# Kernel optimization log

Hardware: AMD Instinct MI355X
Metric: run time of the kernel (lower is better)

Reference implementation:

```python
import jax, jax.numpy as jnp
import numpy as np

STATE_DIM = 64
HIDDEN_DIM = 256
BATCH = 4096
DT = 0.01


def setup_inputs() -> dict:
    key = jax.random.key(0)
    ks = jax.random.split(key, 7)
    s = 1.0 / np.sqrt(STATE_DIM)
    h = 1.0 / np.sqrt(HIDDEN_DIM)
    return {
        "x0": jax.random.normal(ks[0], (BATCH, STATE_DIM), dtype=jnp.float32),
        "W1": jax.random.uniform(ks[1], (STATE_DIM, HIDDEN_DIM), jnp.float32, -s, s),
        "b1": jax.random.uniform(ks[2], (HIDDEN_DIM,), jnp.float32, -s, s),
        "W2": jax.random.uniform(ks[3], (HIDDEN_DIM, HIDDEN_DIM), jnp.float32, -h, h),
        "b2": jax.random.uniform(ks[4], (HIDDEN_DIM,), jnp.float32, -h, h),
        "W3": jax.random.uniform(ks[5], (HIDDEN_DIM, STATE_DIM), jnp.float32, -h, h),
        "b3": jax.random.uniform(ks[6], (STATE_DIM,), jnp.float32, -h, h),
        "dt_scale": jnp.ones((1,), dtype=jnp.float32) * 0.01,
        "steps": 200,
    }


def reference(x0, W1, b1, W2, b2, W3, b3, dt_scale, steps):
    def func(x):
        h1 = jnp.tanh(x @ W1 + b1)
        h2 = jnp.tanh(h1 @ W2 + b2)
        return h2 @ W3 + b3

    def step(x, _):
        x_next = x + func(x) * dt_scale * DT  # Euler update
        return x_next, x_next

    _, traj = jax.lax.scan(step, x0, None, length=steps)
    # traj: [steps, batch, state_dim] -> [batch, steps+1, state_dim]
    return jnp.concatenate([x0[:, None, :], jnp.swapaxes(traj, 0, 1)], axis=1)
```

## Files before the change

kernel.cpp:

```cpp
#include <hip/hip_runtime.h>


#define STATE_DIM 64
#define HIDDEN    256
#define BATCH     4096
#define TILE_M    16
#define NBLK      (BATCH / TILE_M)
#define XPITCH    72
#define HPITCH    264

typedef short v8s __attribute__((ext_vector_type(8)));
typedef float v4f __attribute__((ext_vector_type(4)));

__device__ __forceinline__ unsigned short f2bf(float f) {
    unsigned u = __float_as_uint(f);
    u += 0x7fffu + ((u >> 16) & 1u);
    return (unsigned short)(u >> 16);
}

__device__ __forceinline__ float fast_tanh(float x) {
    float e = __builtin_amdgcn_exp2f(x * 2.8853900817779268f);
    return 1.0f - 2.0f * __builtin_amdgcn_rcpf(e + 1.0f);
}

__global__ void prep_weights(const float* __restrict__ W1,
                             const float* __restrict__ W2,
                             const float* __restrict__ W3,
                             short* __restrict__ W1t,
                             short* __restrict__ W2t,
                             short* __restrict__ W3t) {
    int u = blockIdx.x * 256 + threadIdx.x;
    if (u < 65536) {
        int n = u >> 8, k = u & 255;
        W2t[u] = (short)f2bf(W2[k * 256 + n]);
    }
    int v = u - 65536;
    if (v >= 0 && v < 16384) {
        int n = v >> 6, k = v & 63;
        W1t[v] = (short)f2bf(W1[k * 256 + n]);
    }
    int t = u - (65536 + 16384);
    if (t >= 0 && t < 16384) {
        int n = t >> 8, k = t & 255;
        W3t[t] = (short)f2bf(W3[k * 64 + n]);
    }
}

__global__ __launch_bounds__(512, 2)
void ode_kernel(const float* __restrict__ x0,
                const float* __restrict__ b1,
                const float* __restrict__ b2,
                const float* __restrict__ b3,
                const float* __restrict__ dt_scale,
                const int*   __restrict__ stepsp,
                const short* __restrict__ W1t,
                const short* __restrict__ W2t,
                const short* __restrict__ W3t,
                float* __restrict__ out) {
    __shared__ float xs[TILE_M * STATE_DIM];
    __shared__ short xb[TILE_M * XPITCH];
    __shared__ short h1b[TILE_M * HPITCH];
    __shared__ short h2b[TILE_M * HPITCH];

    const int tid  = threadIdx.x;
    const int w    = tid >> 6;
    const int lane = tid & 63;
    const int ln   = lane & 15;
    const int q    = lane >> 4;
    const int blk  = blockIdx.x;
    const int nsteps = *stepsp;
    const float scale = dt_scale[0] * 0.01f;

    v8s w1f[2][2], w2f[2][8], w3f[8];
    const int n0 = 32 * w;
    #pragma unroll
    for (int t = 0; t < 2; t++)
        #pragma unroll
        for (int s = 0; s < 2; s++)
            w1f[t][s] = *(const v8s*)(W1t + (n0 + 16 * t + ln) * 64 + 32 * s + 8 * q);
    #pragma unroll
    for (int t = 0; t < 2; t++)
        #pragma unroll
        for (int s = 0; s < 8; s++)
            w2f[t][s] = *(const v8s*)(W2t + (n0 + 16 * t + ln) * 256 + 32 * s + 8 * q);
    if (w < 4) {
        #pragma unroll
        for (int s = 0; s < 8; s++)
            w3f[s] = *(const v8s*)(W3t + (16 * w + ln) * 256 + 32 * s + 8 * q);
    }
    float b1r[2], b2r[2], b3r = 0.0f;
    #pragma unroll
    for (int t = 0; t < 2; t++) {
        b1r[t] = b1[n0 + 16 * t + ln];
        b2r[t] = b2[n0 + 16 * t + ln];
    }
    if (w < 4) b3r = b3[16 * w + ln];

    {
        int r = tid >> 5, c = (tid & 31) * 2;
        const float2 v = *(const float2*)(x0 + (size_t)(blk * TILE_M + r) * STATE_DIM + c);
        xs[r * STATE_DIM + c]     = v.x;
        xs[r * STATE_DIM + c + 1] = v.y;
        xb[r * XPITCH + c]     = (short)f2bf(v.x);
        xb[r * XPITCH + c + 1] = (short)f2bf(v.y);
    }
    __syncthreads();

    const size_t orow = (size_t)(nsteps + 1) * STATE_DIM;

    for (int s = 0; s <= nsteps; s++) {
        {
            int r = tid >> 5, c = (tid & 31) * 2;
            float2 v;
            v.x = xs[r * STATE_DIM + c];
            v.y = xs[r * STATE_DIM + c + 1];
            *(float2*)(out + (size_t)(blk * TILE_M + r) * orow + (size_t)s * STATE_DIM + c) = v;
        }
        if (s == nsteps) break;

        v4f acc0 = {0.f, 0.f, 0.f, 0.f}, acc1 = {0.f, 0.f, 0.f, 0.f};
        #pragma unroll
        for (int ks = 0; ks < 2; ks++) {
            v8s a = *(const v8s*)(xb + ln * XPITCH + 32 * ks + 8 * q);
            acc0 = __builtin_amdgcn_mfma_f32_16x16x32_bf16(a, w1f[0][ks], acc0, 0, 0, 0);
            acc1 = __builtin_amdgcn_mfma_f32_16x16x32_bf16(a, w1f[1][ks], acc1, 0, 0, 0);
        }
        #pragma unroll
        for (int i = 0; i < 4; i++) {
            int row = q * 4 + i;
            h1b[row * HPITCH + n0 + ln]      = (short)f2bf(fast_tanh(acc0[i] + b1r[0]));
            h1b[row * HPITCH + n0 + 16 + ln] = (short)f2bf(fast_tanh(acc1[i] + b1r[1]));
        }
        __syncthreads();

        acc0 = (v4f){0.f, 0.f, 0.f, 0.f};
        acc1 = (v4f){0.f, 0.f, 0.f, 0.f};
        #pragma unroll
        for (int ks = 0; ks < 8; ks++) {
            v8s a = *(const v8s*)(h1b + ln * HPITCH + 32 * ks + 8 * q);
            acc0 = __builtin_amdgcn_mfma_f32_16x16x32_bf16(a, w2f[0][ks], acc0, 0, 0, 0);
            acc1 = __builtin_amdgcn_mfma_f32_16x16x32_bf16(a, w2f[1][ks], acc1, 0, 0, 0);
        }
        #pragma unroll
        for (int i = 0; i < 4; i++) {
            int row = q * 4 + i;
            h2b[row * HPITCH + n0 + ln]      = (short)f2bf(fast_tanh(acc0[i] + b2r[0]));
            h2b[row * HPITCH + n0 + 16 + ln] = (short)f2bf(fast_tanh(acc1[i] + b2r[1]));
        }
        __syncthreads();

        if (w < 4) {
            v4f acc = {0.f, 0.f, 0.f, 0.f};
            #pragma unroll
            for (int ks = 0; ks < 8; ks++) {
                v8s a = *(const v8s*)(h2b + ln * HPITCH + 32 * ks + 8 * q);
                acc = __builtin_amdgcn_mfma_f32_16x16x32_bf16(a, w3f[ks], acc, 0, 0, 0);
            }
            #pragma unroll
            for (int i = 0; i < 4; i++) {
                int row = q * 4 + i;
                int col = 16 * w + ln;
                float xn = xs[row * STATE_DIM + col] + (acc[i] + b3r) * scale;
                xs[row * STATE_DIM + col] = xn;
                xb[row * XPITCH + col]    = (short)f2bf(xn);
            }
        }
        __syncthreads();
    }
}

extern "C" void kernel_launch(void* const* d_in, const int* in_sizes, int n_in,
                              void* d_out, int out_size, void* d_ws, size_t ws_size,
                              hipStream_t stream) {
    const float* x0 = (const float*)d_in[0];
    const float* W1 = (const float*)d_in[1];
    const float* b1 = (const float*)d_in[2];
    const float* W2 = (const float*)d_in[3];
    const float* b2 = (const float*)d_in[4];
    const float* W3 = (const float*)d_in[5];
    const float* b3 = (const float*)d_in[6];
    const float* dt = (const float*)d_in[7];
    const int* steps = (const int*)d_in[8];

    short* W1t = (short*)d_ws;
    short* W2t = W1t + 64 * 256;
    short* W3t = W2t + 256 * 256;

    prep_weights<<<384, 256, 0, stream>>>(W1, W2, W3, W1t, W2t, W3t);
    ode_kernel<<<NBLK, 512, 0, stream>>>(x0, b1, b2, b3, dt, steps,
                                         W1t, W2t, W3t, (float*)d_out);
}
```

Before: 453.1 us.

## Use 1024-thread blocks with swizzled LDS, W3 in LDS, and overlapped trajectory stores

```diff
diff --git a/kernel.cpp b/kernel.cpp
--- a/kernel.cpp
+++ b/kernel.cpp
@@ -3,19 +3,14 @@
 
 #define STATE_DIM 64
 #define HIDDEN    256
-#define BATCH     4096
 #define TILE_M    16
-#define NBLK      (BATCH / TILE_M)
-#define XPITCH    72
-#define HPITCH    264
+#define NBLK      256
 
 typedef short v8s __attribute__((ext_vector_type(8)));
 typedef float v4f __attribute__((ext_vector_type(4)));
 
 __device__ __forceinline__ unsigned short f2bf(float f) {
-    unsigned u = __float_as_uint(f);
-    u += 0x7fffu + ((u >> 16) & 1u);
-    return (unsigned short)(u >> 16);
+    return (unsigned short)((__float_as_uint(f) + 0x8000u) >> 16);
 }
 
 __device__ __forceinline__ float fast_tanh(float x) {
@@ -46,7 +41,7 @@
     }
 }
 
-__global__ __launch_bounds__(512, 2)
+__global__ __launch_bounds__(1024)
 void ode_kernel(const float* __restrict__ x0,
                 const float* __restrict__ b1,
                 const float* __restrict__ b2,
@@ -57,10 +52,11 @@
                 const short* __restrict__ W2t,
                 const short* __restrict__ W3t,
                 float* __restrict__ out) {
-    __shared__ float xs[TILE_M * STATE_DIM];
-    __shared__ short xb[TILE_M * XPITCH];
-    __shared__ short h1b[TILE_M * HPITCH];
-    __shared__ short h2b[TILE_M * HPITCH];
+    __shared__ short h1b[TILE_M * HIDDEN];
+    __shared__ short h2b[TILE_M * HIDDEN];
+    __shared__ short xb [TILE_M * STATE_DIM];
+    __shared__ short w3s[STATE_DIM * HIDDEN];
+    __shared__ float xs [2][TILE_M * 65];
 
     const int tid  = threadIdx.x;
     const int w    = tid >> 6;
@@ -70,102 +66,125 @@
     const int blk  = blockIdx.x;
     const int nsteps = *stepsp;
     const float scale = dt_scale[0] * 0.01f;
-
-    v8s w1f[2][2], w2f[2][8], w3f[8];
-    const int n0 = 32 * w;
-    #pragma unroll
-    for (int t = 0; t < 2; t++)
-        #pragma unroll
-        for (int s = 0; s < 2; s++)
-            w1f[t][s] = *(const v8s*)(W1t + (n0 + 16 * t + ln) * 64 + 32 * s + 8 * q);
-    #pragma unroll
-    for (int t = 0; t < 2; t++)
-        #pragma unroll
-        for (int s = 0; s < 8; s++)
-            w2f[t][s] = *(const v8s*)(W2t + (n0 + 16 * t + ln) * 256 + 32 * s + 8 * q);
-    if (w < 4) {
-        #pragma unroll
-        for (int s = 0; s < 8; s++)
-            w3f[s] = *(const v8s*)(W3t + (16 * w + ln) * 256 + 32 * s + 8 * q);
-    }
-    float b1r[2], b2r[2], b3r = 0.0f;
-    #pragma unroll
-    for (int t = 0; t < 2; t++) {
-        b1r[t] = b1[n0 + 16 * t + ln];
-        b2r[t] = b2[n0 + 16 * t + ln];
-    }
-    if (w < 4) b3r = b3[16 * w + ln];
-
+    const int n0 = 16 * w;
+
+    v8s w1f[2], w2f[8];
+    #pragma unroll
+    for (int ks = 0; ks < 2; ks++)
+        w1f[ks] = *(const v8s*)(W1t + (n0 + ln) * 64 + 32 * ks + 8 * q);
+    #pragma unroll
+    for (int ks = 0; ks < 8; ks++)
+        w2f[ks] = *(const v8s*)(W2t + (n0 + ln) * 256 + 32 * ks + 8 * q);
+    const float b1r = b1[n0 + ln];
+    const float b2r = b2[n0 + ln];
+    const float b3r = b3[16 * (w & 3) + ln];
+
+    #pragma unroll
+    for (int c2 = 0; c2 < 2; c2++) {
+        int u = c2 * 1024 + tid;
+        int r = u >> 5, cb = u & 31;
+        v8s v = *(const v8s*)(W3t + r * 256 + cb * 8);
+        *(v8s*)(w3s + r * 256 + ((cb ^ (r & 7)) << 3)) = v;
+    }
     {
-        int r = tid >> 5, c = (tid & 31) * 2;
-        const float2 v = *(const float2*)(x0 + (size_t)(blk * TILE_M + r) * STATE_DIM + c);
-        xs[r * STATE_DIM + c]     = v.x;
-        xs[r * STATE_DIM + c + 1] = v.y;
-        xb[r * XPITCH + c]     = (short)f2bf(v.x);
-        xb[r * XPITCH + c + 1] = (short)f2bf(v.y);
+        float v = x0[(size_t)(blk * TILE_M + w) * STATE_DIM + lane];
+        xs[0][w * 65 + lane] = v;
+        xb[w * 64 + (((lane >> 3) ^ (w & 7)) << 3) + (lane & 7)] = (short)f2bf(v);
     }
     __syncthreads();
 
+    int hrd[8], hwr[4], xrd[2], w3rd[8], xwr[4], xsi[4];
+    #pragma unroll
+    for (int ks = 0; ks < 8; ks++)
+        hrd[ks] = ln * 256 + (((4 * ks + q) ^ (ln & 7)) << 3);
+    #pragma unroll
+    for (int ks = 0; ks < 2; ks++)
+        xrd[ks] = ln * 64 + (((4 * ks + q) ^ (ln & 7)) << 3);
+    #pragma unroll
+    for (int i = 0; i < 4; i++) {
+        int r = 4 * q + i, c = n0 + ln;
+        hwr[i] = r * 256 + (((c >> 3) ^ (r & 7)) << 3) + (c & 7);
+    }
+    {
+        int r3 = 16 * (w & 3) + ln;
+        #pragma unroll
+        for (int ks = 0; ks < 8; ks++)
+            w3rd[ks] = r3 * 256 + (((4 * ks + q) ^ (r3 & 7)) << 3);
+        #pragma unroll
+        for (int i = 0; i < 4; i++) {
+            int r = 4 * q + i, c = 16 * (w & 3) + ln;
+            xwr[i] = r * 64 + (((c >> 3) ^ (r & 7)) << 3) + (c & 7);
+            xsi[i] = r * 65 + c;
+        }
+    }
+
     const size_t orow = (size_t)(nsteps + 1) * STATE_DIM;
-
-    for (int s = 0; s <= nsteps; s++) {
-        {
-            int r = tid >> 5, c = (tid & 31) * 2;
-            float2 v;
-            v.x = xs[r * STATE_DIM + c];
-            v.y = xs[r * STATE_DIM + c + 1];
-            *(float2*)(out + (size_t)(blk * TILE_M + r) * orow + (size_t)s * STATE_DIM + c) = v;
-        }
-        if (s == nsteps) break;
-
-        v4f acc0 = {0.f, 0.f, 0.f, 0.f}, acc1 = {0.f, 0.f, 0.f, 0.f};
+    float* tp1 = out;
+    float* tp2 = out;
+    int xsr1 = 0, xsr2 = 0;
+    if (w >= 4) {
+        tp1  = out + (size_t)(blk * TILE_M + (w - 4)) * orow + lane;
+        xsr1 = (w - 4) * 65 + lane;
+    }
+    if (w >= 4 && w < 8) {
+        tp2  = out + (size_t)(blk * TILE_M + (w + 8)) * orow + lane;
+        xsr2 = (w + 8) * 65 + lane;
+    }
+
+    for (int s = 0; s < nsteps; s++) {
+        const int cur = s & 1, nxt = cur ^ 1;
+
+        v4f acc = {0.f, 0.f, 0.f, 0.f};
         #pragma unroll
         for (int ks = 0; ks < 2; ks++) {
-            v8s a = *(const v8s*)(xb + ln * XPITCH + 32 * ks + 8 * q);
-            acc0 = __builtin_amdgcn_mfma_f32_16x16x32_bf16(a, w1f[0][ks], acc0, 0, 0, 0);
-            acc1 = __builtin_amdgcn_mfma_f32_16x16x32_bf16(a, w1f[1][ks], acc1, 0, 0, 0);
-        }
-        #pragma unroll
-        for (int i = 0; i < 4; i++) {
-            int row = q * 4 + i;
-            h1b[row * HPITCH + n0 + ln]      = (short)f2bf(fast_tanh(acc0[i] + b1r[0]));
-            h1b[row * HPITCH + n0 + 16 + ln] = (short)f2bf(fast_tanh(acc1[i] + b1r[1]));
-        }
+            v8s a = *(const v8s*)(xb + xrd[ks]);
+            acc = __builtin_amdgcn_mfma_f32_16x16x32_bf16(a, w1f[ks], acc, 0, 0, 0);
+        }
+        #pragma unroll
+        for (int i = 0; i < 4; i++)
+            h1b[hwr[i]] = (short)f2bf(fast_tanh(acc[i] + b1r));
         __syncthreads();
 
-        acc0 = (v4f){0.f, 0.f, 0.f, 0.f};
-        acc1 = (v4f){0.f, 0.f, 0.f, 0.f};
+        acc = (v4f){0.f, 0.f, 0.f, 0.f};
         #pragma unroll
         for (int ks = 0; ks < 8; ks++) {
-            v8s a = *(const v8s*)(h1b + ln * HPITCH + 32 * ks + 8 * q);
-            acc0 = __builtin_amdgcn_mfma_f32_16x16x32_bf16(a, w2f[0][ks], acc0, 0, 0, 0);
-            acc1 = __builtin_amdgcn_mfma_f32_16x16x32_bf16(a, w2f[1][ks], acc1, 0, 0, 0);
-        }
-        #pragma unroll
-        for (int i = 0; i < 4; i++) {
-            int row = q * 4 + i;
-            h2b[row * HPITCH + n0 + ln]      = (short)f2bf(fast_tanh(acc0[i] + b2r[0]));
-            h2b[row * HPITCH + n0 + 16 + ln] = (short)f2bf(fast_tanh(acc1[i] + b2r[1]));
-        }
+            v8s a = *(const v8s*)(h1b + hrd[ks]);
+            acc = __builtin_amdgcn_mfma_f32_16x16x32_bf16(a, w2f[ks], acc, 0, 0, 0);
+        }
+        #pragma unroll
+        for (int i = 0; i < 4; i++)
+            h2b[hwr[i]] = (short)f2bf(fast_tanh(acc[i] + b2r));
         __syncthreads();
 
         if (w < 4) {
-            v4f acc = {0.f, 0.f, 0.f, 0.f};
+            v4f a3 = {0.f, 0.f, 0.f, 0.f};
             #pragma unroll
             for (int ks = 0; ks < 8; ks++) {
-                v8s a = *(const v8s*)(h2b + ln * HPITCH + 32 * ks + 8 * q);
-                acc = __builtin_amdgcn_mfma_f32_16x16x32_bf16(a, w3f[ks], acc, 0, 0, 0);
+                v8s a = *(const v8s*)(h2b + hrd[ks]);
+                v8s b = *(const v8s*)(w3s + w3rd[ks]);
+                a3 = __builtin_amdgcn_mfma_f32_16x16x32_bf16(a, b, a3, 0, 0, 0);
             }
             #pragma unroll
             for (int i = 0; i < 4; i++) {
-                int row = q * 4 + i;
-                int col = 16 * w + ln;
-                float xn = xs[row * STATE_DIM + col] + (acc[i] + b3r) * scale;
-                xs[row * STATE_DIM + col] = xn;
-                xb[row * XPITCH + col]    = (short)f2bf(xn);
+                float xo = xs[cur][xsi[i]];
+                float xn = xo + (a3[i] + b3r) * scale;
+                xs[nxt][xsi[i]] = xn;
+                xb[xwr[i]] = (short)f2bf(xn);
             }
+        } else {
+            *tp1 = xs[cur][xsr1];
+            tp1 += STATE_DIM;
+            if (w < 8) {
+                *tp2 = xs[cur][xsr2];
+                tp2 += STATE_DIM;
+            }
         }
         __syncthreads();
+    }
+
+    {
+        float v = xs[nsteps & 1][w * 65 + lane];
+        out[(size_t)(blk * TILE_M + w) * orow + (size_t)nsteps * STATE_DIM + lane] = v;
     }
 }
 
@@ -187,6 +206,6 @@
     short* W3t = W2t + 256 * 256;
 
     prep_weights<<<384, 256, 0, stream>>>(W1, W2, W3, W1t, W2t, W3t);
-    ode_kernel<<<NBLK, 512, 0, stream>>>(x0, b1, b2, b3, dt, steps,
-                                         W1t, W2t, W3t, (float*)d_out);
-}
+    ode_kernel<<<NBLK, 1024, 0, stream>>>(x0, b1, b2, b3, dt, steps,
+                                          W1t, W2t, W3t, (float*)d_out);
+}
```

Result: slower. 472.8 us (+4.4%).

## Overlap trajectory stores with layer-3 compute using double-buffered state

Applied to the files above, without the earlier changes.

```diff
diff --git a/kernel.cpp b/kernel.cpp
--- a/kernel.cpp
+++ b/kernel.cpp
@@ -3,19 +3,17 @@
 
 #define STATE_DIM 64
 #define HIDDEN    256
-#define BATCH     4096
 #define TILE_M    16
-#define NBLK      (BATCH / TILE_M)
+#define NBLK      256
 #define XPITCH    72
 #define HPITCH    264
+#define XSP       68
 
 typedef short v8s __attribute__((ext_vector_type(8)));
 typedef float v4f __attribute__((ext_vector_type(4)));
 
 __device__ __forceinline__ unsigned short f2bf(float f) {
-    unsigned u = __float_as_uint(f);
-    u += 0x7fffu + ((u >> 16) & 1u);
-    return (unsigned short)(u >> 16);
+    return (unsigned short)((__float_as_uint(f) + 0x8000u) >> 16);
 }
 
 __device__ __forceinline__ float fast_tanh(float x) {
@@ -57,10 +55,10 @@
                 const short* __restrict__ W2t,
                 const short* __restrict__ W3t,
                 float* __restrict__ out) {
-    __shared__ float xs[TILE_M * STATE_DIM];
-    __shared__ short xb[TILE_M * XPITCH];
+    __shared__ short xb [TILE_M * XPITCH];
     __shared__ short h1b[TILE_M * HPITCH];
     __shared__ short h2b[TILE_M * HPITCH];
+    __shared__ float xs [2][TILE_M * XSP];
 
     const int tid  = threadIdx.x;
     const int w    = tid >> 6;
@@ -70,23 +68,23 @@
     const int blk  = blockIdx.x;
     const int nsteps = *stepsp;
     const float scale = dt_scale[0] * 0.01f;
+    const int n0 = 32 * w;
 
     v8s w1f[2][2], w2f[2][8], w3f[8];
-    const int n0 = 32 * w;
     #pragma unroll
     for (int t = 0; t < 2; t++)
         #pragma unroll
-        for (int s = 0; s < 2; s++)
-            w1f[t][s] = *(const v8s*)(W1t + (n0 + 16 * t + ln) * 64 + 32 * s + 8 * q);
+        for (int ks = 0; ks < 2; ks++)
+            w1f[t][ks] = *(const v8s*)(W1t + (n0 + 16 * t + ln) * 64 + 32 * ks + 8 * q);
     #pragma unroll
     for (int t = 0; t < 2; t++)
         #pragma unroll
-        for (int s = 0; s < 8; s++)
-            w2f[t][s] = *(const v8s*)(W2t + (n0 + 16 * t + ln) * 256 + 32 * s + 8 * q);
+        for (int ks = 0; ks < 8; ks++)
+            w2f[t][ks] = *(const v8s*)(W2t + (n0 + 16 * t + ln) * 256 + 32 * ks + 8 * q);
     if (w < 4) {
         #pragma unroll
-        for (int s = 0; s < 8; s++)
-            w3f[s] = *(const v8s*)(W3t + (16 * w + ln) * 256 + 32 * s + 8 * q);
+        for (int ks = 0; ks < 8; ks++)
+            w3f[ks] = *(const v8s*)(W3t + (16 * w + ln) * 256 + 32 * ks + 8 * q);
     }
     float b1r[2], b2r[2], b3r = 0.0f;
     #pragma unroll
@@ -99,73 +97,107 @@
     {
         int r = tid >> 5, c = (tid & 31) * 2;
         const float2 v = *(const float2*)(x0 + (size_t)(blk * TILE_M + r) * STATE_DIM + c);
-        xs[r * STATE_DIM + c]     = v.x;
-        xs[r * STATE_DIM + c + 1] = v.y;
+        xs[0][r * XSP + c]     = v.x;
+        xs[0][r * XSP + c + 1] = v.y;
         xb[r * XPITCH + c]     = (short)f2bf(v.x);
         xb[r * XPITCH + c + 1] = (short)f2bf(v.y);
     }
     __syncthreads();
 
+    int xrd[2], hrd[8], hw0, xsU[4], xbU[4];
+    #pragma unroll
+    for (int ks = 0; ks < 2; ks++) xrd[ks] = ln * XPITCH + 32 * ks + 8 * q;
+    #pragma unroll
+    for (int ks = 0; ks < 8; ks++) hrd[ks] = ln * HPITCH + 32 * ks + 8 * q;
+    hw0 = (4 * q) * HPITCH + n0 + ln;
+    {
+        int col = 16 * (w & 3) + ln;
+        #pragma unroll
+        for (int i = 0; i < 4; i++) {
+            xsU[i] = (4 * q + i) * XSP + col;
+            xbU[i] = (4 * q + i) * XPITCH + col;
+        }
+    }
+
     const size_t orow = (size_t)(nsteps + 1) * STATE_DIM;
-
-    for (int s = 0; s <= nsteps; s++) {
-        {
-            int r = tid >> 5, c = (tid & 31) * 2;
-            float2 v;
-            v.x = xs[r * STATE_DIM + c];
-            v.y = xs[r * STATE_DIM + c + 1];
-            *(float2*)(out + (size_t)(blk * TILE_M + r) * orow + (size_t)s * STATE_DIM + c) = v;
-        }
-        if (s == nsteps) break;
-
+    float* tp[4];
+    int trd[4];
+    {
+        int r0 = 4 * (w - 4);
+        #pragma unroll
+        for (int j = 0; j < 4; j++) {
+            int r = (w >= 4) ? (r0 + j) : 0;
+            tp[j]  = out + (size_t)(blk * TILE_M + r) * orow + lane;
+            trd[j] = r * XSP + lane;
+        }
+    }
+
+    for (int s = 0; s < nsteps; s++) {
+        const int cur = s & 1, nxt = cur ^ 1;
+
+        v8s xa0 = *(const v8s*)(xb + xrd[0]);
+        v8s xa1 = *(const v8s*)(xb + xrd[1]);
         v4f acc0 = {0.f, 0.f, 0.f, 0.f}, acc1 = {0.f, 0.f, 0.f, 0.f};
-        #pragma unroll
-        for (int ks = 0; ks < 2; ks++) {
-            v8s a = *(const v8s*)(xb + ln * XPITCH + 32 * ks + 8 * q);
-            acc0 = __builtin_amdgcn_mfma_f32_16x16x32_bf16(a, w1f[0][ks], acc0, 0, 0, 0);
-            acc1 = __builtin_amdgcn_mfma_f32_16x16x32_bf16(a, w1f[1][ks], acc1, 0, 0, 0);
-        }
+        acc0 = __builtin_amdgcn_mfma_f32_16x16x32_bf16(xa0, w1f[0][0], acc0, 0, 0, 0);
+        acc1 = __builtin_amdgcn_mfma_f32_16x16x32_bf16(xa0, w1f[1][0], acc1, 0, 0, 0);
+        acc0 = __builtin_amdgcn_mfma_f32_16x16x32_bf16(xa1, w1f[0][1], acc0, 0, 0, 0);
+        acc1 = __builtin_amdgcn_mfma_f32_16x16x32_bf16(xa1, w1f[1][1], acc1, 0, 0, 0);
         #pragma unroll
         for (int i = 0; i < 4; i++) {
-            int row = q * 4 + i;
-            h1b[row * HPITCH + n0 + ln]      = (short)f2bf(fast_tanh(acc0[i] + b1r[0]));
-            h1b[row * HPITCH + n0 + 16 + ln] = (short)f2bf(fast_tanh(acc1[i] + b1r[1]));
+            h1b[hw0 + i * HPITCH]      = (short)f2bf(fast_tanh(acc0[i] + b1r[0]));
+            h1b[hw0 + i * HPITCH + 16] = (short)f2bf(fast_tanh(acc1[i] + b1r[1]));
         }
         __syncthreads();
 
+        v8s a[8];
+        #pragma unroll
+        for (int ks = 0; ks < 8; ks++) a[ks] = *(const v8s*)(h1b + hrd[ks]);
         acc0 = (v4f){0.f, 0.f, 0.f, 0.f};
         acc1 = (v4f){0.f, 0.f, 0.f, 0.f};
         #pragma unroll
         for (int ks = 0; ks < 8; ks++) {
-            v8s a = *(const v8s*)(h1b + ln * HPITCH + 32 * ks + 8 * q);
-            acc0 = __builtin_amdgcn_mfma_f32_16x16x32_bf16(a, w2f[0][ks], acc0, 0, 0, 0);
-            acc1 = __builtin_amdgcn_mfma_f32_16x16x32_bf16(a, w2f[1][ks], acc1, 0, 0, 0);
+            acc0 = __builtin_amdgcn_mfma_f32_16x16x32_bf16(a[ks], w2f[0][ks], acc0, 0, 0, 0);
+            acc1 = __builtin_amdgcn_mfma_f32_16x16x32_bf16(a[ks], w2f[1][ks], acc1, 0, 0, 0);
         }
         #pragma unroll
         for (int i = 0; i < 4; i++) {
-            int row = q * 4 + i;
-            h2b[row * HPITCH + n0 + ln]      = (short)f2bf(fast_tanh(acc0[i] + b2r[0]));
-            h2b[row * HPITCH + n0 + 16 + ln] = (short)f2bf(fast_tanh(acc1[i] + b2r[1]));
+            h2b[hw0 + i * HPITCH]      = (short)f2bf(fast_tanh(acc0[i] + b2r[0]));
+            h2b[hw0 + i * HPITCH + 16] = (short)f2bf(fast_tanh(acc1[i] + b2r[1]));
         }
         __syncthreads();
 
         if (w < 4) {
-            v4f acc = {0.f, 0.f, 0.f, 0.f};
-            #pragma unroll
-            for (int ks = 0; ks < 8; ks++) {
-                v8s a = *(const v8s*)(h2b + ln * HPITCH + 32 * ks + 8 * q);
-                acc = __builtin_amdgcn_mfma_f32_16x16x32_bf16(a, w3f[ks], acc, 0, 0, 0);
+            v8s c[8];
+            #pragma unroll
+            for (int ks = 0; ks < 8; ks++) c[ks] = *(const v8s*)(h2b + hrd[ks]);
+            v4f a3 = {0.f, 0.f, 0.f, 0.f};
+            #pragma unroll
+            for (int ks = 0; ks < 8; ks++)
+                a3 = __builtin_amdgcn_mfma_f32_16x16x32_bf16(c[ks], w3f[ks], a3, 0, 0, 0);
+            #pragma unroll
+            for (int i = 0; i < 4; i++) {
+                float xn = xs[cur][xsU[i]] + (a3[i] + b3r) * scale;
+                xs[nxt][xsU[i]] = xn;
+                xb[xbU[i]] = (short)f2bf(xn);
             }
-            #pragma unroll
-            for (int i = 0; i < 4; i++) {
-                int row = q * 4 + i;
-                int col = 16 * w + ln;
-                float xn = xs[row * STATE_DIM + col] + (acc[i] + b3r) * scale;
-                xs[row * STATE_DIM + col] = xn;
-                xb[row * XPITCH + col]    = (short)f2bf(xn);
+        } else {
+            #pragma unroll
+            for (int j = 0; j < 4; j++) {
+                *tp[j] = xs[cur][trd[j]];
+                tp[j] += STATE_DIM;
             }
         }
         __syncthreads();
+    }
+
+    {
+        const float* xsf = xs[nsteps & 1];
+        #pragma unroll
+        for (int j = 0; j < 2; j++) {
+            int r = 2 * w + j;
+            out[(size_t)(blk * TILE_M + r) * orow + (size_t)nsteps * STATE_DIM + lane] =
+                xsf[r * XSP + lane];
+        }
     }
 }
 
```

Result: no change. 448.5 us (-1.0%).
